# Kernel tuning notes

Measured on AMD Instinct MI355X. Metric: run time of the kernel, lower is better.

## Reference

```python
import jax, jax.numpy as jnp
import numpy as np

WINDOW = 8
HEADS = 16
HIDDEN = 256
EMBED = HIDDEN * WINDOW          # 2048
HEAD_DIM = EMBED // HEADS        # 128
BATCH = 8
SEQ = 4096                       # multiple of WINDOW
GROUP = SEQ // WINDOW            # 512


def _indices():
    # index_one[i*g + j] = j*w + i  (residue-class grouping permutation)
    i = np.arange(WINDOW)
    j = np.arange(GROUP)
    index_one = (j[None, :] * WINDOW + i[:, None]).reshape(-1)
    # index_two[i*w + k] = k*g + i  (inverse-style interleave permutation)
    index_two = (np.arange(WINDOW)[None, :] * GROUP + np.arange(GROUP)[:, None]).reshape(-1)
    return jnp.asarray(index_one), jnp.asarray(index_two)


def _attention(M, Wq, Wk, Wv, fc_w, fc_b):
    # M: [N, g, E] with E = heads*head_dim
    N, L, E = M.shape
    x = M.reshape(N, L, HEADS, HEAD_DIM)
    q = jnp.einsum('nlhd,ed->nlhe', x, Wq)
    k = jnp.einsum('nlhd,ed->nlhe', x, Wk)
    v = jnp.einsum('nlhd,ed->nlhe', x, Wv)
    energy = jnp.einsum('nqhd,nkhd->nhqk', q, k)
    attn = jax.nn.softmax(energy / jnp.sqrt(jnp.float32(EMBED)), axis=-1)
    out = jnp.einsum('nhqk,nkhd->nqhd', attn, v).reshape(N, L, E)
    return out @ fc_w.T + fc_b


def setup_inputs() -> dict:
    key = jax.random.key(0)
    ks = jax.random.split(key, 6)
    s = 0.02
    return {
        'M': jax.random.normal(ks[0], (BATCH, SEQ, HIDDEN), jnp.float32),
        'Wq': jax.random.normal(ks[1], (HEAD_DIM, HEAD_DIM), jnp.float32) * s,
        'Wk': jax.random.normal(ks[2], (HEAD_DIM, HEAD_DIM), jnp.float32) * s,
        'Wv': jax.random.normal(ks[3], (HEAD_DIM, HEAD_DIM), jnp.float32) * s,
        'fc_w': jax.random.normal(ks[4], (EMBED, EMBED), jnp.float32) * s,
        'fc_b': jax.random.normal(ks[5], (EMBED,), jnp.float32) * s,
        'device': 0,
    }


def reference(M, Wq, Wk, Wv, fc_w, fc_b, device):
    del device  # unused, mirrors torch signature
    index_one, index_two = _indices()
    N, S, H = M.shape
    w, g = WINDOW, GROUP
    for b in range(w):
        idx = (index_one - b) % S
        M = M[:, idx]                                             # gather permute
        # segmentation step 1: [N, w*g, H] -> [N, g, w*H]
        M = M.reshape(N, w, g, H).transpose(0, 2, 1, 3).reshape(N, g, w * H)
        M = _attention(M, Wq, Wk, Wv, fc_w, fc_b)
        # segmentation step 2: [N, g, w*H] -> [N, w*g, H]
        M = M.reshape(N, g, w, H).transpose(0, 2, 1, 3).reshape(N, w * g, H)
        # index_two rotated once per iteration after the first -> roll by -b
        M = M[:, jnp.roll(index_two, -b)]
    return M[:, :S]
```

## Files before the change

### kernel.cpp

```cpp
#include <hip/hip_runtime.h>
#include <stdint.h>

typedef unsigned short u16;
typedef unsigned int u32;
typedef __bf16 bf16x8 __attribute__((ext_vector_type(8)));
typedef float f32x4 __attribute__((ext_vector_type(4)));
typedef float f32x16 __attribute__((ext_vector_type(16)));
typedef u16 u16x4 __attribute__((ext_vector_type(4)));
typedef u16 u16x8 __attribute__((ext_vector_type(8)));

#define MFMA16(a, b, c) __builtin_amdgcn_mfma_f32_16x16x32_bf16(a, b, c, 0, 0, 0)
#define MFMA32(a, b, c) __builtin_amdgcn_mfma_f32_32x32x16_bf16(a, b, c, 0, 0, 0)

__device__ __forceinline__ u16 f2bf(float f) {
  u32 u = __builtin_bit_cast(u32, f);
  u += 0x7FFFu + ((u >> 16) & 1u);
  return (u16)(u >> 16);
}

__device__ __forceinline__ bf16x8 ld16(const u16* p) {
  return __builtin_bit_cast(bf16x8, *(const uint4*)p);
}

__device__ __forceinline__ void gl_lds(const u16* src, u16* lds) {
  __builtin_amdgcn_global_load_lds(
      (const __attribute__((address_space(1))) u32*)src,
      (__attribute__((address_space(3))) u32*)lds, 16, 0, 0);
}

__global__ __launch_bounds__(256) void convert_weights(
    const float* __restrict__ Wq, const float* __restrict__ Wk,
    const float* __restrict__ Wv, const float* __restrict__ fcw,
    const float* __restrict__ M, u16* __restrict__ wq_b,
    u16* __restrict__ wk_b, u16* __restrict__ wv_b, u16* __restrict__ fcw_b,
    u16* __restrict__ Sb) {
  int bx = blockIdx.x, tid = threadIdx.x;
  if (bx < 4096) {
    int i = (bx * 256 + tid) * 4;
    float4 f = *(const float4*)&fcw[i];
    u16x4 o = {f2bf(f.x), f2bf(f.y), f2bf(f.z), f2bf(f.w)};
    *(u16x4*)&fcw_b[i] = o;
  } else if (bx < 4112) {
    int i = ((bx - 4096) * 256 + tid) * 4;
    const float sc = 0.022097086912079612f;
    float4 q = *(const float4*)&Wq[i];
    u16x4 oq = {f2bf(q.x * sc), f2bf(q.y * sc), f2bf(q.z * sc), f2bf(q.w * sc)};
    *(u16x4*)&wq_b[i] = oq;
    float4 k = *(const float4*)&Wk[i];
    u16x4 ok = {f2bf(k.x), f2bf(k.y), f2bf(k.z), f2bf(k.w)};
    *(u16x4*)&wk_b[i] = ok;
    float4 v = *(const float4*)&Wv[i];
    u16x4 ov = {f2bf(v.x), f2bf(v.y), f2bf(v.z), f2bf(v.w)};
    *(u16x4*)&wv_b[i] = ov;
  } else {
    size_t i = ((size_t)(bx - 4112) * 256 + tid) * 8;
    float4 f0 = *(const float4*)&M[i];
    float4 f1 = *(const float4*)&M[i + 4];
    u16x8 v = {f2bf(f0.x), f2bf(f0.y), f2bf(f0.z), f2bf(f0.w),
               f2bf(f1.x), f2bf(f1.y), f2bf(f1.z), f2bf(f1.w)};
    *(u16x8*)&Sb[i] = v;
  }
}

__global__ __launch_bounds__(512) void kv_kernel(
    const u16* __restrict__ srcB, const u16* __restrict__ wk,
    const u16* __restrict__ wvw, u16* __restrict__ K, u16* __restrict__ Vt,
    int bsh) {
  __shared__ u16 X[64 * 264];
  int jt = blockIdx.x, i0 = blockIdx.y, n = blockIdx.z;
  int tid = threadIdx.x;
#pragma unroll
  for (int it = 0; it < 4; ++it) {
    int c = tid + it * 512;
    int row = c >> 5, seg = c & 31;
    int pos = (8 * (jt * 64 + row) + i0 - bsh) & 4095;
    size_t base = ((size_t)n * 4096 + pos) * 256 + seg * 8;
    *(u16x8*)&X[row * 264 + seg * 8] = *(const u16x8*)&srcB[base];
  }
  __syncthreads();
  int wvid = tid >> 6, ln = tid & 63;
  int mat = wvid >> 2, hc = wvid & 3;
  int hh = hc >> 1, cb = (hc & 1) * 64;
  int h = i0 * 2 + hh, xc = hh * 128;
  const u16* W = (mat == 0) ? wk : wvw;
  int lr = ln & 15, lg = ln >> 4;
  f32x4 acc[4][4] = {};
#pragma unroll
  for (int kt = 0; kt < 4; ++kt) {
    bf16x8 a[4], b[4];
#pragma unroll
    for (int mt = 0; mt < 4; ++mt)
      a[mt] = ld16(&X[(mt * 16 + lr) * 264 + xc + kt * 32 + lg * 8]);
#pragma unroll
    for (int nc = 0; nc < 4; ++nc)
      b[nc] = ld16(&W[(cb + nc * 16 + lr) * 128 + kt * 32 + lg * 8]);
#pragma unroll
    for (int mt = 0; mt < 4; ++mt)
#pragma unroll
      for (int nc = 0; nc < 4; ++nc)
        acc[mt][nc] = MFMA16(a[mt], b[nc], acc[mt][nc]);
  }
  size_t nh = (size_t)(n * 16 + h);
  if (mat == 0) {
    u16* dst = K + nh * 512 * 128;
#pragma unroll
    for (int mt = 0; mt < 4; ++mt)
#pragma unroll
      for (int nc = 0; nc < 4; ++nc) {
        int col = cb + nc * 16 + lr;
        int jb = jt * 64 + mt * 16 + lg * 4;
#pragma unroll
        for (int r = 0; r < 4; ++r)
          dst[(size_t)(jb + r) * 128 + col] = f2bf(acc[mt][nc][r]);
      }
  } else {
    u16* dst = Vt + nh * 128 * 512;
#pragma unroll
    for (int mt = 0; mt < 4; ++mt)
#pragma unroll
      for (int nc = 0; nc < 4; ++nc) {
        int col = cb + nc * 16 + lr;
        int jb = jt * 64 + mt * 16 + lg * 4;
        u16x4 pk = {f2bf(acc[mt][nc][0]), f2bf(acc[mt][nc][1]),
                    f2bf(acc[mt][nc][2]), f2bf(acc[mt][nc][3])};
        *(u16x4*)&dst[(size_t)col * 512 + jb] = pk;
      }
  }
}

__global__ __launch_bounds__(256, 2) void attn_kernel(
    const u16* __restrict__ Sb, const u16* __restrict__ wq,
    const u16* __restrict__ K, const u16* __restrict__ Vt,
    u16* __restrict__ O, int bsh) {
  __shared__ u16 SMEM[40960];
#define KLp(b) (&SMEM[(b) * 8192])
#define VLp(b) (&SMEM[24576 + (b) * 8192])
  int flat = blockIdx.x;
  int xcd = flat & 7, idx = flat >> 3;
  int gl = idx & 15, qt = idx >> 4;
  int g = xcd | (gl << 3);
  int h = g & 15, n = g >> 4;
  int tid = threadIdx.x, wv = tid >> 6, ln = tid & 63;
  int l31 = ln & 31, hh = ln >> 5;
  size_t nh = (size_t)(n * 16 + h);
  int q0 = qt * 128 + wv * 32;
  const u16* Kb = K + (size_t)nh * 512 * 128;
  const u16* Vb = Vt + (size_t)nh * 128 * 512;
  int i0h = h >> 1, c0 = (h & 1) * 128;

#pragma unroll
  for (int i = 0; i < 8; ++i) {
    int s = wv * 8 + i;
    int r = 4 * s + (ln >> 4);
    int slot = (ln & 15) ^ (r & 15);
    int pos = (8 * (qt * 128 + r) + i0h - bsh) & 4095;
    gl_lds(&Sb[((size_t)n * 4096 + pos) * 256 + c0 + slot * 8], &SMEM[s * 512]);
    gl_lds(&wq[r * 128 + slot * 8], &SMEM[16384 + s * 512]);
  }
  __syncthreads();
  f32x16 qd[4] = {};
  int jr = wv * 32 + l31;
#pragma unroll
  for (int cs = 0; cs < 8; ++cs) {
    bf16x8 xf = ld16(&SMEM[jr * 128 + ((2 * cs + hh) ^ (jr & 15)) * 8]);
#pragma unroll
    for (int eb = 0; eb < 4; ++eb) {
      int er = eb * 32 + l31;
      bf16x8 wf = ld16(&SMEM[16384 + er * 128 + ((2 * cs + hh) ^ (er & 15)) * 8]);
      qd[eb] = MFMA32(wf, xf, qd[eb]);
    }
  }
  bf16x8 qf[8];
#pragma unroll
  for (int kt = 0; kt < 8; ++kt) {
    const int eb = kt >> 1, r0 = 8 * (kt & 1);
    u32 wA, wB, wC, wD;
    asm("v_cvt_pk_bf16_f32 %0, %1, %2" : "=v"(wA) : "v"(qd[eb][r0 + 0]), "v"(qd[eb][r0 + 1]));
    asm("v_cvt_pk_bf16_f32 %0, %1, %2" : "=v"(wB) : "v"(qd[eb][r0 + 2]), "v"(qd[eb][r0 + 3]));
    asm("v_cvt_pk_bf16_f32 %0, %1, %2" : "=v"(wC) : "v"(qd[eb][r0 + 4]), "v"(qd[eb][r0 + 5]));
    asm("v_cvt_pk_bf16_f32 %0, %1, %2" : "=v"(wD) : "v"(qd[eb][r0 + 6]), "v"(qd[eb][r0 + 7]));
    asm("v_permlane32_swap_b32 %0, %1" : "+v"(wA), "+v"(wC));
    asm("v_permlane32_swap_b32 %0, %1" : "+v"(wB), "+v"(wD));
    uint4 ww = {wA, wB, wC, wD};
    qf[kt] = __builtin_bit_cast(bf16x8, ww);
  }
  __syncthreads();

  int l16 = ln & 15, l8 = ln & 7;
  int rK[4], cK[4], rV[4], cV[4];
#pragma unroll
  for (int i = 0; i < 4; ++i) {
    int s = wv * 4 + i;
    rK[i] = 4 * s + (ln >> 4);
    cK[i] = (l16 ^ (rK[i] & 15)) * 8;
    rV[i] = 8 * s + (ln >> 3);
    cV[i] = (l8 ^ (rV[i] & 7)) * 8;
  }

#define STAGE_K(buf, kv)                                                     \
  {                                                                          \
    const u16* kp_ = Kb + (size_t)(kv) * 64 * 128;                           \
    _Pragma("unroll") for (int i_ = 0; i_ < 4; ++i_) {                       \
      int s_ = wv * 4 + i_;                                                  \
      gl_lds(&kp_[(size_t)rK[i_] * 128 + cK[i_]], &KLp(buf)[s_ * 512]);      \
    }                                                                        \
  }
#define STAGE_V(buf, kv)                                                     \
  {                                                                          \
    _Pragma("unroll") for (int i_ = 0; i_ < 4; ++i_) {                       \
      int s_ = wv * 4 + i_;                                                  \
      gl_lds(&Vb[(size_t)rV[i_] * 512 + (kv)*64 + cV[i_]], &VLp(buf)[s_ * 512]); \
    }                                                                        \
  }

  STAGE_K(0, 0);
  STAGE_V(0, 0);
  STAGE_K(1, 1);
  __syncthreads();

  f32x16 ps[2][2];
  f32x16 o[4] = {};
  float m = -1e30f, l = 0.f;

  {
    f32x16 z = {};
    ps[0][0] = z; ps[0][1] = z;
#pragma unroll
    for (int kt = 0; kt < 8; ++kt) {
      int slot0 = (2 * kt + hh) ^ (l31 & 15);
      bf16x8 a0 = ld16(&KLp(0)[l31 * 128 + slot0 * 8]);
      ps[0][0] = MFMA32(a0, qf[kt], ps[0][0]);
      int row1 = 32 + l31;
      int slot1 = (2 * kt + hh) ^ (row1 & 15);
      bf16x8 a1 = ld16(&KLp(0)[row1 * 128 + slot1 * 8]);
      ps[0][1] = MFMA32(a1, qf[kt], ps[0][1]);
    }
  }

#pragma unroll
  for (int t = 0; t < 8; ++t) {
    const int cur = t & 1, nxt = (t + 1) & 1;
    if (t + 2 <= 7) STAGE_K((t + 2) % 3, t + 2);
    if (t + 1 <= 7) STAGE_V(nxt, t + 1);
    if (t + 1 <= 7) {
      const int kb = (t + 1) % 3;
      f32x16 z = {};
      ps[nxt][0] = z; ps[nxt][1] = z;
#pragma unroll
      for (int kt = 0; kt < 8; ++kt) {
        int slot0 = (2 * kt + hh) ^ (l31 & 15);
        bf16x8 a0 = ld16(&KLp(kb)[l31 * 128 + slot0 * 8]);
        ps[nxt][0] = MFMA32(a0, qf[kt], ps[nxt][0]);
        int row1 = 32 + l31;
        int slot1 = (2 * kt + hh) ^ (row1 & 15);
        bf16x8 a1 = ld16(&KLp(kb)[row1 * 128 + slot1 * 8]);
        ps[nxt][1] = MFMA32(a1, qf[kt], ps[nxt][1]);
      }
    }
    float mx[8];
#pragma unroll
    for (int i = 0; i < 8; ++i)
      mx[i] = fmaxf(fmaxf(ps[cur][0][2 * i], ps[cur][0][2 * i + 1]),
                    fmaxf(ps[cur][1][2 * i], ps[cur][1][2 * i + 1]));
    float pm = fmaxf(fmaxf(fmaxf(mx[0], mx[1]), fmaxf(mx[2], mx[3])),
                     fmaxf(fmaxf(mx[4], mx[5]), fmaxf(mx[6], mx[7])));
    pm = fmaxf(pm, __shfl_xor(pm, 32));
    if (!__all(pm <= m + 8.f)) {
      float nm = fmaxf(m, pm);
      float al = __expf(m - nm);
      l *= al;
      m = nm;
#pragma unroll
      for (int r = 0; r < 16; ++r) {
        int qr = (r & 3) + 8 * (r >> 2) + 4 * hh;
        float av = __shfl(al, (ln & 32) | qr, 64);
        o[0][r] *= av; o[1][r] *= av; o[2][r] *= av; o[3][r] *= av;
      }
    }
#pragma unroll
    for (int kb2 = 0; kb2 < 2; ++kb2)
#pragma unroll
      for (int r = 0; r < 16; ++r)
        ps[cur][kb2][r] = __expf(ps[cur][kb2][r] - m);
    float sm[8];
#pragma unroll
    for (int i = 0; i < 8; ++i)
      sm[i] = (ps[cur][0][2 * i] + ps[cur][0][2 * i + 1]) +
              (ps[cur][1][2 * i] + ps[cur][1][2 * i + 1]);
    float rs = ((sm[0] + sm[1]) + (sm[2] + sm[3])) +
               ((sm[4] + sm[5]) + (sm[6] + sm[7]));
    rs += __shfl_xor(rs, 32);
    l += rs;
    bf16x8 pa[4];
#pragma unroll
    for (int ks = 0; ks < 4; ++ks) {
      const int kb2 = ks >> 1, r0 = 8 * (ks & 1);
      u32 wA, wB, wC, wD;
      asm("v_cvt_pk_bf16_f32 %0, %1, %2" : "=v"(wA) : "v"(ps[cur][kb2][r0 + 0]), "v"(ps[cur][kb2][r0 + 1]));
      asm("v_cvt_pk_bf16_f32 %0, %1, %2" : "=v"(wB) : "v"(ps[cur][kb2][r0 + 2]), "v"(ps[cur][kb2][r0 + 3]));
      asm("v_cvt_pk_bf16_f32 %0, %1, %2" : "=v"(wC) : "v"(ps[cur][kb2][r0 + 4]), "v"(ps[cur][kb2][r0 + 5]));
      asm("v_cvt_pk_bf16_f32 %0, %1, %2" : "=v"(wD) : "v"(ps[cur][kb2][r0 + 6]), "v"(ps[cur][kb2][r0 + 7]));
      asm("v_permlane32_swap_b32 %0, %1" : "+v"(wA), "+v"(wC));
      asm("v_permlane32_swap_b32 %0, %1" : "+v"(wB), "+v"(wD));
      uint4 ww = {wA, wB, wC, wD};
      pa[ks] = __builtin_bit_cast(bf16x8, ww);
    }
    __builtin_amdgcn_s_setprio(1);
#pragma unroll
    for (int ks = 0; ks < 4; ++ks)
#pragma unroll
      for (int nb = 0; nb < 4; ++nb) {
        int row = nb * 32 + l31;
        int slot = (2 * ks + hh) ^ (row & 7);
        bf16x8 bv = ld16(&VLp(cur)[row * 64 + slot * 8]);
        o[nb] = MFMA32(pa[ks], bv, o[nb]);
      }
    __builtin_amdgcn_s_setprio(0);
    if (t < 7) __syncthreads();
  }
#undef STAGE_K
#undef STAGE_V
#undef KLp
#undef VLp

  float inv = 1.f / l;
#pragma unroll
  for (int r = 0; r < 16; ++r) {
    int qr = (r & 3) + 8 * (r >> 2) + 4 * hh;
    float iv = __shfl(inv, (ln & 32) | qr, 64);
    int row = q0 + qr;
    u16* dst = O + ((size_t)n * 512 + row) * 2048 + h * 128;
    dst[0 * 32 + l31] = f2bf(o[0][r] * iv);
    dst[1 * 32 + l31] = f2bf(o[1][r] * iv);
    dst[2 * 32 + l31] = f2bf(o[2][r] * iv);
    dst[3 * 32 + l31] = f2bf(o[3][r] * iv);
  }
}

__global__ __launch_bounds__(512, 1) void fc_kernel(
    const u16* __restrict__ A, const u16* __restrict__ Bw,
    const float* __restrict__ bias, float* __restrict__ doutF,
    u16* __restrict__ doutB, int last, int bsh) {
  __shared__ u16 AL[3][256 * 64];
  __shared__ u16 BL[3][128 * 64];
  int blk = blockIdx.x;
  int xcd = blk & 7, j = blk >> 3;
  int bn = xcd * 2 + (j & 1), bm = j >> 1;
  int tid = threadIdx.x, wv = tid >> 6, ln = tid & 63;
  int lr = ln & 15, lg = ln >> 4;
  int R0 = bm * 256, C0 = bn * 128;
  int wr = (wv >> 1) * 64, wc = (wv & 1) * 64;
  const u16* gA[4];
  int sA[4];
  const u16* gB[2];
  int sB[2];
#pragma unroll
  for (int i = 0; i < 4; ++i) {
    int r = wv * 32 + i * 8 + (ln >> 3);
    int cs = ((ln & 7) ^ (r & 7)) * 8;
    gA[i] = A + (size_t)(R0 + r) * 2048 + cs;
    sA[i] = (wv * 32 + i * 8) * 64;
  }
#pragma unroll
  for (int i = 0; i < 2; ++i) {
    int r = wv * 16 + i * 8 + (ln >> 3);
    int cs = ((ln & 7) ^ (r & 7)) * 8;
    gB[i] = Bw + (size_t)(C0 + r) * 2048 + cs;
    sB[i] = (wv * 16 + i * 8) * 64;
  }
  int aoff[4][2], boff[4][2];
#pragma unroll
  for (int i = 0; i < 4; ++i) {
    int ra = wr + i * 16 + lr, rb = wc + i * 16 + lr;
#pragma unroll
    for (int kk = 0; kk < 2; ++kk) {
      aoff[i][kk] = ra * 64 + (((kk * 4 + lg) ^ (ra & 7)) * 8);
      boff[i][kk] = rb * 64 + (((kk * 4 + lg) ^ (rb & 7)) * 8);
    }
  }
  f32x4 acc[4][4] = {};

#define STAGE6(buf, k0)                          \
  {                                              \
    gl_lds(gA[0] + (k0), &AL[buf][sA[0]]);       \
    gl_lds(gA[1] + (k0), &AL[buf][sA[1]]);       \
    gl_lds(gA[2] + (k0), &AL[buf][sA[2]]);       \
    gl_lds(gA[3] + (k0), &AL[buf][sA[3]]);       \
    gl_lds(gB[0] + (k0), &BL[buf][sB[0]]);       \
    gl_lds(gB[1] + (k0), &BL[buf][sB[1]]);       \
  }

  STAGE6(0, 0);
  STAGE6(1, 64);
  asm volatile("s_waitcnt vmcnt(6)" ::: "memory");
  __builtin_amdgcn_s_barrier();

  for (int t = 0; t < 32; ++t) {
    int cur = t % 3, nx2 = (t + 2) % 3;
    int k2 = (t + 2) * 64;
    bf16x8 a0 = ld16(&AL[cur][aoff[0][0]]), a1 = ld16(&AL[cur][aoff[1][0]]);
    bf16x8 a2 = ld16(&AL[cur][aoff[2][0]]), a3 = ld16(&AL[cur][aoff[3][0]]);
    bf16x8 b0 = ld16(&BL[cur][boff[0][0]]), b1 = ld16(&BL[cur][boff[1][0]]);
    bf16x8 b2 = ld16(&BL[cur][boff[2][0]]), b3 = ld16(&BL[cur][boff[3][0]]);
    if (t < 30) {
      gl_lds(gA[0] + k2, &AL[nx2][sA[0]]);
      gl_lds(gA[1] + k2, &AL[nx2][sA[1]]);
      gl_lds(gB[0] + k2, &BL[nx2][sB[0]]);
    }
    __builtin_amdgcn_s_barrier();
    asm volatile("s_waitcnt lgkmcnt(0)" ::: "memory");
    __builtin_amdgcn_sched_barrier(0);
    __builtin_amdgcn_s_setprio(1);
    acc[0][0] = MFMA16(a0, b0, acc[0][0]);
    acc[0][1] = MFMA16(a0, b1, acc[0][1]);
    acc[0][2] = MFMA16(a0, b2, acc[0][2]);
    acc[0][3] = MFMA16(a0, b3, acc[0][3]);
    acc[1][0] = MFMA16(a1, b0, acc[1][0]);
    acc[1][1] = MFMA16(a1, b1, acc[1][1]);
    acc[1][2] = MFMA16(a1, b2, acc[1][2]);
    acc[1][3] = MFMA16(a1, b3, acc[1][3]);
    acc[2][0] = MFMA16(a2, b0, acc[2][0]);
    acc[2][1] = MFMA16(a2, b1, acc[2][1]);
    acc[2][2] = MFMA16(a2, b2, acc[2][2]);
    acc[2][3] = MFMA16(a2, b3, acc[2][3]);
    acc[3][0] = MFMA16(a3, b0, acc[3][0]);
    acc[3][1] = MFMA16(a3, b1, acc[3][1]);
    acc[3][2] = MFMA16(a3, b2, acc[3][2]);
    acc[3][3] = MFMA16(a3, b3, acc[3][3]);
    __builtin_amdgcn_s_setprio(0);
    __builtin_amdgcn_s_barrier();
    a0 = ld16(&AL[cur][aoff[0][1]]); a1 = ld16(&AL[cur][aoff[1][1]]);
    a2 = ld16(&AL[cur][aoff[2][1]]); a3 = ld16(&AL[cur][aoff[3][1]]);
    b0 = ld16(&BL[cur][boff[0][1]]); b1 = ld16(&BL[cur][boff[1][1]]);
    b2 = ld16(&BL[cur][boff[2][1]]); b3 = ld16(&BL[cur][boff[3][1]]);
    if (t < 30) {
      gl_lds(gA[2] + k2, &AL[nx2][sA[2]]);
      gl_lds(gA[3] + k2, &AL[nx2][sA[3]]);
      gl_lds(gB[1] + k2, &BL[nx2][sB[1]]);
      asm volatile("s_waitcnt vmcnt(6)" ::: "memory");
    } else if (t == 30) {
      asm volatile("s_waitcnt vmcnt(0)" ::: "memory");
    }
    __builtin_amdgcn_s_barrier();
    asm volatile("s_waitcnt lgkmcnt(0)" ::: "memory");
    __builtin_amdgcn_sched_barrier(0);
    __builtin_amdgcn_s_setprio(1);
    acc[0][0] = MFMA16(a0, b0, acc[0][0]);
    acc[0][1] = MFMA16(a0, b1, acc[0][1]);
    acc[0][2] = MFMA16(a0, b2, acc[0][2]);
    acc[0][3] = MFMA16(a0, b3, acc[0][3]);
    acc[1][0] = MFMA16(a1, b0, acc[1][0]);
    acc[1][1] = MFMA16(a1, b1, acc[1][1]);
    acc[1][2] = MFMA16(a1, b2, acc[1][2]);
    acc[1][3] = MFMA16(a1, b3, acc[1][3]);
    acc[2][0] = MFMA16(a2, b0, acc[2][0]);
    acc[2][1] = MFMA16(a2, b1, acc[2][1]);
    acc[2][2] = MFMA16(a2, b2, acc[2][2]);
    acc[2][3] = MFMA16(a2, b3, acc[2][3]);
    acc[3][0] = MFMA16(a3, b0, acc[3][0]);
    acc[3][1] = MFMA16(a3, b1, acc[3][1]);
    acc[3][2] = MFMA16(a3, b2, acc[3][2]);
    acc[3][3] = MFMA16(a3, b3, acc[3][3]);
    __builtin_amdgcn_s_setprio(0);
    __builtin_amdgcn_s_barrier();
  }
#undef STAGE6
#pragma unroll
  for (int nc = 0; nc < 4; ++nc) {
    int e = C0 + wc + nc * 16 + lr;
    float bv = bias[e];
    int i = e >> 8, cc = e & 255;
#pragma unroll
    for (int mt = 0; mt < 4; ++mt)
#pragma unroll
      for (int r = 0; r < 4; ++r) {
        int row = R0 + wr + mt * 16 + lg * 4 + r;
        int nn = row >> 9, jj = row & 511;
        int pos = (8 * jj + i - bsh) & 4095;
        size_t di = ((size_t)nn * 4096 + pos) * 256 + cc;
        float v = acc[mt][nc][r] + bv;
        if (last) doutF[di] = v;
        else doutB[di] = f2bf(v);
      }
  }
}

extern "C" void kernel_launch(void* const* d_in, const int* in_sizes, int n_in,
                              void* d_out, int out_size, void* d_ws, size_t ws_size,
                              hipStream_t stream) {
  const float* M = (const float*)d_in[0];
  const float* Wq = (const float*)d_in[1];
  const float* Wk = (const float*)d_in[2];
  const float* Wv = (const float*)d_in[3];
  const float* fcw = (const float*)d_in[4];
  const float* fcb = (const float*)d_in[5];
  float* out = (float*)d_out;
  char* ws = (char*)d_ws;
  u16* wq_b = (u16*)(ws + (0 << 10));
  u16* wk_b = (u16*)(ws + (32 << 10));
  u16* wv_b = (u16*)(ws + (64 << 10));
  u16* fcw_b = (u16*)(ws + (128 << 10));
  u16* Kb = (u16*)(ws + ((size_t)32 << 20));
  u16* Vtb = (u16*)(ws + ((size_t)48 << 20));
  u16* Ab = (u16*)(ws + ((size_t)64 << 20));
  u16* Sb = (u16*)(ws + ((size_t)96 << 20));

  convert_weights<<<8208, 256, 0, stream>>>(Wq, Wk, Wv, fcw, M, wq_b, wk_b,
                                            wv_b, fcw_b, Sb);
  for (int b = 0; b < 8; ++b) {
    kv_kernel<<<dim3(8, 8, 8), 512, 0, stream>>>(Sb, wk_b, wv_b, Kb, Vtb, b);
    attn_kernel<<<512, 256, 0, stream>>>(Sb, wq_b, Kb, Vtb, Ab, b);
    fc_kernel<<<256, 512, 0, stream>>>(Ab, fcw_b, fcb, out, Sb,
                                       (b == 7) ? 1 : 0, b);
  }
}
```

Before: 704.6 us.

## Shrink attention LDS footprint to allow three blocks per CU

```diff
diff --git a/kernel.cpp b/kernel.cpp
--- a/kernel.cpp
+++ b/kernel.cpp
@@ -128,13 +128,11 @@
   }
 }
 
-__global__ __launch_bounds__(256, 2) void attn_kernel(
+__global__ __launch_bounds__(256, 3) void attn_kernel(
     const u16* __restrict__ Sb, const u16* __restrict__ wq,
     const u16* __restrict__ K, const u16* __restrict__ Vt,
     u16* __restrict__ O, int bsh) {
-  __shared__ u16 SMEM[40960];
-#define KLp(b) (&SMEM[(b) * 8192])
-#define VLp(b) (&SMEM[24576 + (b) * 8192])
+  __shared__ u16 SMEM[24576];
   int flat = blockIdx.x;
   int xcd = flat & 7, idx = flat >> 3;
   int gl = idx & 15, qt = idx >> 4;
@@ -155,6 +153,12 @@
     int slot = (ln & 15) ^ (r & 15);
     int pos = (8 * (qt * 128 + r) + i0h - bsh) & 4095;
     gl_lds(&Sb[((size_t)n * 4096 + pos) * 256 + c0 + slot * 8], &SMEM[s * 512]);
+  }
+#pragma unroll
+  for (int i = 0; i < 4; ++i) {
+    int s = wv * 4 + i;
+    int r = 4 * s + (ln >> 4);
+    int slot = (ln & 15) ^ (r & 15);
     gl_lds(&wq[r * 128 + slot * 8], &SMEM[16384 + s * 512]);
   }
   __syncthreads();
@@ -164,9 +168,29 @@
   for (int cs = 0; cs < 8; ++cs) {
     bf16x8 xf = ld16(&SMEM[jr * 128 + ((2 * cs + hh) ^ (jr & 15)) * 8]);
 #pragma unroll
-    for (int eb = 0; eb < 4; ++eb) {
+    for (int eb = 0; eb < 2; ++eb) {
       int er = eb * 32 + l31;
       bf16x8 wf = ld16(&SMEM[16384 + er * 128 + ((2 * cs + hh) ^ (er & 15)) * 8]);
+      qd[eb] = MFMA32(wf, xf, qd[eb]);
+    }
+  }
+  __syncthreads();
+#pragma unroll
+  for (int i = 0; i < 4; ++i) {
+    int s = wv * 4 + i;
+    int rg = 64 + 4 * s + (ln >> 4);
+    int slot = (ln & 15) ^ (rg & 15);
+    gl_lds(&wq[rg * 128 + slot * 8], &SMEM[16384 + s * 512]);
+  }
+  __syncthreads();
+#pragma unroll
+  for (int cs = 0; cs < 8; ++cs) {
+    bf16x8 xf = ld16(&SMEM[jr * 128 + ((2 * cs + hh) ^ (jr & 15)) * 8]);
+#pragma unroll
+    for (int eb = 2; eb < 4; ++eb) {
+      int erg = eb * 32 + l31;
+      int loc = erg - 64;
+      bf16x8 wf = ld16(&SMEM[16384 + loc * 128 + ((2 * cs + hh) ^ (erg & 15)) * 8]);
       qd[eb] = MFMA32(wf, xf, qd[eb]);
     }
   }
@@ -197,71 +221,48 @@
     cV[i] = (l8 ^ (rV[i] & 7)) * 8;
   }
 
-#define STAGE_K(buf, kv)                                                     \
-  {                                                                          \
-    const u16* kp_ = Kb + (size_t)(kv) * 64 * 128;                           \
-    _Pragma("unroll") for (int i_ = 0; i_ < 4; ++i_) {                       \
-      int s_ = wv * 4 + i_;                                                  \
-      gl_lds(&kp_[(size_t)rK[i_] * 128 + cK[i_]], &KLp(buf)[s_ * 512]);      \
-    }                                                                        \
-  }
-#define STAGE_V(buf, kv)                                                     \
-  {                                                                          \
-    _Pragma("unroll") for (int i_ = 0; i_ < 4; ++i_) {                       \
-      int s_ = wv * 4 + i_;                                                  \
-      gl_lds(&Vb[(size_t)rV[i_] * 512 + (kv)*64 + cV[i_]], &VLp(buf)[s_ * 512]); \
-    }                                                                        \
+#define STAGE_K(buf, kv)                                                       \
+  {                                                                            \
+    const u16* kp_ = Kb + (size_t)(kv) * 64 * 128;                             \
+    _Pragma("unroll") for (int i_ = 0; i_ < 4; ++i_) {                         \
+      int s_ = wv * 4 + i_;                                                    \
+      gl_lds(&kp_[(size_t)rK[i_] * 128 + cK[i_]], &SMEM[(buf)*8192 + s_ * 512]); \
+    }                                                                          \
+  }
+#define STAGE_V(kv)                                                            \
+  {                                                                            \
+    _Pragma("unroll") for (int i_ = 0; i_ < 4; ++i_) {                         \
+      int s_ = wv * 4 + i_;                                                    \
+      gl_lds(&Vb[(size_t)rV[i_] * 512 + (kv)*64 + cV[i_]], &SMEM[16384 + s_ * 512]); \
+    }                                                                          \
   }
 
   STAGE_K(0, 0);
-  STAGE_V(0, 0);
-  STAGE_K(1, 1);
   __syncthreads();
 
-  f32x16 ps[2][2];
   f32x16 o[4] = {};
   float m = -1e30f, l = 0.f;
 
-  {
-    f32x16 z = {};
-    ps[0][0] = z; ps[0][1] = z;
+  for (int t = 0; t < 8; ++t) {
+    const int cur = t & 1;
+    STAGE_V(t);
+    if (t < 7) STAGE_K(cur ^ 1, t + 1);
+    f32x16 s[2] = {};
 #pragma unroll
     for (int kt = 0; kt < 8; ++kt) {
       int slot0 = (2 * kt + hh) ^ (l31 & 15);
-      bf16x8 a0 = ld16(&KLp(0)[l31 * 128 + slot0 * 8]);
-      ps[0][0] = MFMA32(a0, qf[kt], ps[0][0]);
+      bf16x8 a0 = ld16(&SMEM[cur * 8192 + l31 * 128 + slot0 * 8]);
+      s[0] = MFMA32(a0, qf[kt], s[0]);
       int row1 = 32 + l31;
       int slot1 = (2 * kt + hh) ^ (row1 & 15);
-      bf16x8 a1 = ld16(&KLp(0)[row1 * 128 + slot1 * 8]);
-      ps[0][1] = MFMA32(a1, qf[kt], ps[0][1]);
-    }
-  }
-
-#pragma unroll
-  for (int t = 0; t < 8; ++t) {
-    const int cur = t & 1, nxt = (t + 1) & 1;
-    if (t + 2 <= 7) STAGE_K((t + 2) % 3, t + 2);
-    if (t + 1 <= 7) STAGE_V(nxt, t + 1);
-    if (t + 1 <= 7) {
-      const int kb = (t + 1) % 3;
-      f32x16 z = {};
-      ps[nxt][0] = z; ps[nxt][1] = z;
-#pragma unroll
-      for (int kt = 0; kt < 8; ++kt) {
-        int slot0 = (2 * kt + hh) ^ (l31 & 15);
-        bf16x8 a0 = ld16(&KLp(kb)[l31 * 128 + slot0 * 8]);
-        ps[nxt][0] = MFMA32(a0, qf[kt], ps[nxt][0]);
-        int row1 = 32 + l31;
-        int slot1 = (2 * kt + hh) ^ (row1 & 15);
-        bf16x8 a1 = ld16(&KLp(kb)[row1 * 128 + slot1 * 8]);
-        ps[nxt][1] = MFMA32(a1, qf[kt], ps[nxt][1]);
-      }
+      bf16x8 a1 = ld16(&SMEM[cur * 8192 + row1 * 128 + slot1 * 8]);
+      s[1] = MFMA32(a1, qf[kt], s[1]);
     }
     float mx[8];
 #pragma unroll
     for (int i = 0; i < 8; ++i)
-      mx[i] = fmaxf(fmaxf(ps[cur][0][2 * i], ps[cur][0][2 * i + 1]),
-                    fmaxf(ps[cur][1][2 * i], ps[cur][1][2 * i + 1]));
+      mx[i] = fmaxf(fmaxf(s[0][2 * i], s[0][2 * i + 1]),
+                    fmaxf(s[1][2 * i], s[1][2 * i + 1]));
     float pm = fmaxf(fmaxf(fmaxf(mx[0], mx[1]), fmaxf(mx[2], mx[3])),
                      fmaxf(fmaxf(mx[4], mx[5]), fmaxf(mx[6], mx[7])));
     pm = fmaxf(pm, __shfl_xor(pm, 32));
@@ -280,13 +281,11 @@
 #pragma unroll
     for (int kb2 = 0; kb2 < 2; ++kb2)
 #pragma unroll
-      for (int r = 0; r < 16; ++r)
-        ps[cur][kb2][r] = __expf(ps[cur][kb2][r] - m);
+      for (int r = 0; r < 16; ++r) s[kb2][r] = __expf(s[kb2][r] - m);
     float sm[8];
 #pragma unroll
     for (int i = 0; i < 8; ++i)
-      sm[i] = (ps[cur][0][2 * i] + ps[cur][0][2 * i + 1]) +
-              (ps[cur][1][2 * i] + ps[cur][1][2 * i + 1]);
+      sm[i] = (s[0][2 * i] + s[0][2 * i + 1]) + (s[1][2 * i] + s[1][2 * i + 1]);
     float rs = ((sm[0] + sm[1]) + (sm[2] + sm[3])) +
                ((sm[4] + sm[5]) + (sm[6] + sm[7]));
     rs += __shfl_xor(rs, 32);
@@ -296,15 +295,21 @@
     for (int ks = 0; ks < 4; ++ks) {
       const int kb2 = ks >> 1, r0 = 8 * (ks & 1);
       u32 wA, wB, wC, wD;
-      asm("v_cvt_pk_bf16_f32 %0, %1, %2" : "=v"(wA) : "v"(ps[cur][kb2][r0 + 0]), "v"(ps[cur][kb2][r0 + 1]));
-      asm("v_cvt_pk_bf16_f32 %0, %1, %2" : "=v"(wB) : "v"(ps[cur][kb2][r0 + 2]), "v"(ps[cur][kb2][r0 + 3]));
-      asm("v_cvt_pk_bf16_f32 %0, %1, %2" : "=v"(wC) : "v"(ps[cur][kb2][r0 + 4]), "v"(ps[cur][kb2][r0 + 5]));
-      asm("v_cvt_pk_bf16_f32 %0, %1, %2" : "=v"(wD) : "v"(ps[cur][kb2][r0 + 6]), "v"(ps[cur][kb2][r0 + 7]));
+      asm("v_cvt_pk_bf16_f32 %0, %1, %2" : "=v"(wA) : "v"(s[kb2][r0 + 0]), "v"(s[kb2][r0 + 1]));
+      asm("v_cvt_pk_bf16_f32 %0, %1, %2" : "=v"(wB) : "v"(s[kb2][r0 + 2]), "v"(s[kb2][r0 + 3]));
+      asm("v_cvt_pk_bf16_f32 %0, %1, %2" : "=v"(wC) : "v"(s[kb2][r0 + 4]), "v"(s[kb2][r0 + 5]));
+      asm("v_cvt_pk_bf16_f32 %0, %1, %2" : "=v"(wD) : "v"(s[kb2][r0 + 6]), "v"(s[kb2][r0 + 7]));
       asm("v_permlane32_swap_b32 %0, %1" : "+v"(wA), "+v"(wC));
       asm("v_permlane32_swap_b32 %0, %1" : "+v"(wB), "+v"(wD));
       uint4 ww = {wA, wB, wC, wD};
       pa[ks] = __builtin_bit_cast(bf16x8, ww);
     }
+    if (t < 7) {
+      asm volatile("s_waitcnt vmcnt(4)" ::: "memory");
+    } else {
+      asm volatile("s_waitcnt vmcnt(0)" ::: "memory");
+    }
+    __builtin_amdgcn_s_barrier();
     __builtin_amdgcn_s_setprio(1);
 #pragma unroll
     for (int ks = 0; ks < 4; ++ks)
@@ -312,7 +317,7 @@
       for (int nb = 0; nb < 4; ++nb) {
         int row = nb * 32 + l31;
         int slot = (2 * ks + hh) ^ (row & 7);
-        bf16x8 bv = ld16(&VLp(cur)[row * 64 + slot * 8]);
+        bf16x8 bv = ld16(&SMEM[16384 + row * 64 + slot * 8]);
         o[nb] = MFMA32(pa[ks], bv, o[nb]);
       }
     __builtin_amdgcn_s_setprio(0);
@@ -320,8 +325,6 @@
   }
 #undef STAGE_K
 #undef STAGE_V
-#undef KLp
-#undef VLp
 
   float inv = 1.f / l;
 #pragma unroll
```

New measurement: 768.4 us. +9.0%, slower.

## Restructure attention KV pipeline with early V prefetch and partial vmcnt waits

Applied to the files above, without the earlier changes.

```diff
diff --git a/kernel.cpp b/kernel.cpp
--- a/kernel.cpp
+++ b/kernel.cpp
@@ -148,6 +148,33 @@
   const u16* Vb = Vt + (size_t)nh * 128 * 512;
   int i0h = h >> 1, c0 = (h & 1) * 128;
 
+  int l16 = ln & 15, l8 = ln & 7;
+  int rK[4], cK[4], rV[4], cV[4];
+#pragma unroll
+  for (int i = 0; i < 4; ++i) {
+    int s = wv * 4 + i;
+    rK[i] = 4 * s + (ln >> 4);
+    cK[i] = (l16 ^ (rK[i] & 15)) * 8;
+    rV[i] = 8 * s + (ln >> 3);
+    cV[i] = (l8 ^ (rV[i] & 7)) * 8;
+  }
+
+#define STAGE_K(buf, kv)                                                     \
+  {                                                                          \
+    const u16* kp_ = Kb + (size_t)(kv) * 64 * 128;                           \
+    _Pragma("unroll") for (int i_ = 0; i_ < 4; ++i_) {                       \
+      int s_ = wv * 4 + i_;                                                  \
+      gl_lds(&kp_[(size_t)rK[i_] * 128 + cK[i_]], &KLp(buf)[s_ * 512]);      \
+    }                                                                        \
+  }
+#define STAGE_V(buf, kv)                                                     \
+  {                                                                          \
+    _Pragma("unroll") for (int i_ = 0; i_ < 4; ++i_) {                       \
+      int s_ = wv * 4 + i_;                                                  \
+      gl_lds(&Vb[(size_t)rV[i_] * 512 + (kv)*64 + cV[i_]], &VLp(buf)[s_ * 512]); \
+    }                                                                        \
+  }
+
 #pragma unroll
   for (int i = 0; i < 8; ++i) {
     int s = wv * 8 + i;
@@ -157,6 +184,7 @@
     gl_lds(&Sb[((size_t)n * 4096 + pos) * 256 + c0 + slot * 8], &SMEM[s * 512]);
     gl_lds(&wq[r * 128 + slot * 8], &SMEM[16384 + s * 512]);
   }
+  STAGE_V(1, 0);
   __syncthreads();
   f32x16 qd[4] = {};
   int jr = wv * 32 + l31;
@@ -186,82 +214,33 @@
   }
   __syncthreads();
 
-  int l16 = ln & 15, l8 = ln & 7;
-  int rK[4], cK[4], rV[4], cV[4];
-#pragma unroll
-  for (int i = 0; i < 4; ++i) {
-    int s = wv * 4 + i;
-    rK[i] = 4 * s + (ln >> 4);
-    cK[i] = (l16 ^ (rK[i] & 15)) * 8;
-    rV[i] = 8 * s + (ln >> 3);
-    cV[i] = (l8 ^ (rV[i] & 7)) * 8;
-  }
-
-#define STAGE_K(buf, kv)                                                     \
-  {                                                                          \
-    const u16* kp_ = Kb + (size_t)(kv) * 64 * 128;                           \
-    _Pragma("unroll") for (int i_ = 0; i_ < 4; ++i_) {                       \
-      int s_ = wv * 4 + i_;                                                  \
-      gl_lds(&kp_[(size_t)rK[i_] * 128 + cK[i_]], &KLp(buf)[s_ * 512]);      \
-    }                                                                        \
-  }
-#define STAGE_V(buf, kv)                                                     \
-  {                                                                          \
-    _Pragma("unroll") for (int i_ = 0; i_ < 4; ++i_) {                       \
-      int s_ = wv * 4 + i_;                                                  \
-      gl_lds(&Vb[(size_t)rV[i_] * 512 + (kv)*64 + cV[i_]], &VLp(buf)[s_ * 512]); \
-    }                                                                        \
-  }
-
   STAGE_K(0, 0);
-  STAGE_V(0, 0);
   STAGE_K(1, 1);
   __syncthreads();
 
-  f32x16 ps[2][2];
   f32x16 o[4] = {};
   float m = -1e30f, l = 0.f;
 
-  {
-    f32x16 z = {};
-    ps[0][0] = z; ps[0][1] = z;
+#pragma unroll
+  for (int t = 0; t < 8; ++t) {
+    if (t < 7) STAGE_V(t & 1, t + 1);
+    if (t < 6) STAGE_K((t + 2) % 3, t + 2);
+    f32x16 s[2] = {};
 #pragma unroll
     for (int kt = 0; kt < 8; ++kt) {
       int slot0 = (2 * kt + hh) ^ (l31 & 15);
-      bf16x8 a0 = ld16(&KLp(0)[l31 * 128 + slot0 * 8]);
-      ps[0][0] = MFMA32(a0, qf[kt], ps[0][0]);
+      bf16x8 a0 = ld16(&KLp(t % 3)[l31 * 128 + slot0 * 8]);
+      s[0] = MFMA32(a0, qf[kt], s[0]);
       int row1 = 32 + l31;
       int slot1 = (2 * kt + hh) ^ (row1 & 15);
-      bf16x8 a1 = ld16(&KLp(0)[row1 * 128 + slot1 * 8]);
-      ps[0][1] = MFMA32(a1, qf[kt], ps[0][1]);
-    }
-  }
-
-#pragma unroll
-  for (int t = 0; t < 8; ++t) {
-    const int cur = t & 1, nxt = (t + 1) & 1;
-    if (t + 2 <= 7) STAGE_K((t + 2) % 3, t + 2);
-    if (t + 1 <= 7) STAGE_V(nxt, t + 1);
-    if (t + 1 <= 7) {
-      const int kb = (t + 1) % 3;
-      f32x16 z = {};
-      ps[nxt][0] = z; ps[nxt][1] = z;
-#pragma unroll
-      for (int kt = 0; kt < 8; ++kt) {
-        int slot0 = (2 * kt + hh) ^ (l31 & 15);
-        bf16x8 a0 = ld16(&KLp(kb)[l31 * 128 + slot0 * 8]);
-        ps[nxt][0] = MFMA32(a0, qf[kt], ps[nxt][0]);
-        int row1 = 32 + l31;
-        int slot1 = (2 * kt + hh) ^ (row1 & 15);
-        bf16x8 a1 = ld16(&KLp(kb)[row1 * 128 + slot1 * 8]);
-        ps[nxt][1] = MFMA32(a1, qf[kt], ps[nxt][1]);
-      }
+      bf16x8 a1 = ld16(&KLp(t % 3)[row1 * 128 + slot1 * 8]);
+      s[1] = MFMA32(a1, qf[kt], s[1]);
     }
     float mx[8];
 #pragma unroll
     for (int i = 0; i < 8; ++i)
-      mx[i] = fmaxf(fmaxf(ps[cur][0][2 * i], ps[cur][0][2 * i + 1]),
-                    fmaxf(ps[cur][1][2 * i], ps[cur][1][2 * i + 1]));
+      mx[i] = fmaxf(fmaxf(s[0][2 * i], s[0][2 * i + 1]),
+                    fmaxf(s[1][2 * i], s[1][2 * i + 1]));
     float pm = fmaxf(fmaxf(fmaxf(mx[0], mx[1]), fmaxf(mx[2], mx[3])),
                      fmaxf(fmaxf(mx[4], mx[5]), fmaxf(mx[6], mx[7])));
     pm = fmaxf(pm, __shfl_xor(pm, 32));
@@ -280,13 +259,11 @@
 #pragma unroll
     for (int kb2 = 0; kb2 < 2; ++kb2)
 #pragma unroll
-      for (int r = 0; r < 16; ++r)
-        ps[cur][kb2][r] = __expf(ps[cur][kb2][r] - m);
+      for (int r = 0; r < 16; ++r) s[kb2][r] = __expf(s[kb2][r] - m);
     float sm[8];
 #pragma unroll
     for (int i = 0; i < 8; ++i)
-      sm[i] = (ps[cur][0][2 * i] + ps[cur][0][2 * i + 1]) +
-              (ps[cur][1][2 * i] + ps[cur][1][2 * i + 1]);
+      sm[i] = (s[0][2 * i] + s[0][2 * i + 1]) + (s[1][2 * i] + s[1][2 * i + 1]);
     float rs = ((sm[0] + sm[1]) + (sm[2] + sm[3])) +
                ((sm[4] + sm[5]) + (sm[6] + sm[7]));
     rs += __shfl_xor(rs, 32);
@@ -296,10 +273,10 @@
     for (int ks = 0; ks < 4; ++ks) {
       const int kb2 = ks >> 1, r0 = 8 * (ks & 1);
       u32 wA, wB, wC, wD;
-      asm("v_cvt_pk_bf16_f32 %0, %1, %2" : "=v"(wA) : "v"(ps[cur][kb2][r0 + 0]), "v"(ps[cur][kb2][r0 + 1]));
-      asm("v_cvt_pk_bf16_f32 %0, %1, %2" : "=v"(wB) : "v"(ps[cur][kb2][r0 + 2]), "v"(ps[cur][kb2][r0 + 3]));
-      asm("v_cvt_pk_bf16_f32 %0, %1, %2" : "=v"(wC) : "v"(ps[cur][kb2][r0 + 4]), "v"(ps[cur][kb2][r0 + 5]));
-      asm("v_cvt_pk_bf16_f32 %0, %1, %2" : "=v"(wD) : "v"(ps[cur][kb2][r0 + 6]), "v"(ps[cur][kb2][r0 + 7]));
+      asm("v_cvt_pk_bf16_f32 %0, %1, %2" : "=v"(wA) : "v"(s[kb2][r0 + 0]), "v"(s[kb2][r0 + 1]));
+      asm("v_cvt_pk_bf16_f32 %0, %1, %2" : "=v"(wB) : "v"(s[kb2][r0 + 2]), "v"(s[kb2][r0 + 3]));
+      asm("v_cvt_pk_bf16_f32 %0, %1, %2" : "=v"(wC) : "v"(s[kb2][r0 + 4]), "v"(s[kb2][r0 + 5]));
+      asm("v_cvt_pk_bf16_f32 %0, %1, %2" : "=v"(wD) : "v"(s[kb2][r0 + 6]), "v"(s[kb2][r0 + 7]));
       asm("v_permlane32_swap_b32 %0, %1" : "+v"(wA), "+v"(wC));
       asm("v_permlane32_swap_b32 %0, %1" : "+v"(wB), "+v"(wD));
       uint4 ww = {wA, wB, wC, wD};
@@ -312,11 +289,17 @@
       for (int nb = 0; nb < 4; ++nb) {
         int row = nb * 32 + l31;
         int slot = (2 * ks + hh) ^ (row & 7);
-        bf16x8 bv = ld16(&VLp(cur)[row * 64 + slot * 8]);
+        bf16x8 bv = ld16(&VLp((t + 1) & 1)[row * 64 + slot * 8]);
         o[nb] = MFMA32(pa[ks], bv, o[nb]);
       }
     __builtin_amdgcn_s_setprio(0);
-    if (t < 7) __syncthreads();
+    if (t < 6) {
+      asm volatile("s_waitcnt vmcnt(4)" ::: "memory");
+      __builtin_amdgcn_s_barrier();
+    } else if (t == 6) {
+      asm volatile("s_waitcnt vmcnt(0)" ::: "memory");
+      __builtin_amdgcn_s_barrier();
+    }
   }
 #undef STAGE_K
 #undef STAGE_V
```

After: 706.8 us. About the same (+0.3%).
